# Kernel optimization log

Measured on AMD Instinct MI355X. Metric: run time of the kernel, lower is better.

The kernel has to match this reference:

```python
import jax, jax.numpy as jnp
import numpy as np

K = 3
STRIDE = 1
PAD = 1


def conv2d(x, w, b):
    # standard NCHW conv, stride 1, pad 1
    out = jax.lax.conv_general_dilated(
        x, w, (STRIDE, STRIDE), [(PAD, PAD), (PAD, PAD)],
        dimension_numbers=("NCHW", "OIHW", "NCHW"))
    return out + b[None, :, None, None]


def deform_conv2d(x, offset, mask, weight):
    # torchvision.ops.deform_conv2d semantics (offset_groups=1):
    # offset: [B, 2*K*K, Ho, Wo] laid out as (k, (y, x)) per kernel tap k (row-major)
    # mask:   [B, K*K, Ho, Wo]
    B, C, H, W = x.shape
    KK = K * K
    Ho, Wo = offset.shape[2:]
    off = offset.reshape(B, KK, 2, Ho, Wo)

    # base sampling positions: p = out*stride - pad + kernel_tap + offset
    tap_y = jnp.repeat(jnp.arange(K, dtype=x.dtype), K)  # [KK]
    tap_x = jnp.tile(jnp.arange(K, dtype=x.dtype), K)    # [KK]
    grid_y = jnp.arange(Ho, dtype=x.dtype) * STRIDE - PAD
    grid_x = jnp.arange(Wo, dtype=x.dtype) * STRIDE - PAD
    py = grid_y[None, None, :, None] + tap_y[None, :, None, None] + off[:, :, 0]  # [B,KK,Ho,Wo]
    px = grid_x[None, None, None, :] + tap_x[None, :, None, None] + off[:, :, 1]

    y0 = jnp.floor(py)
    x0 = jnp.floor(px)
    wy1 = py - y0  # fractional parts
    wx1 = px - x0

    xf = x.reshape(B, C, H * W)

    def gather(yi, xi):
        # zero-padding semantics: out-of-bounds corners contribute 0
        valid = (yi >= 0) & (yi <= H - 1) & (xi >= 0) & (xi <= W - 1)
        idx = (jnp.clip(yi, 0, H - 1) * W + jnp.clip(xi, 0, W - 1)).astype(jnp.int32)
        v = jnp.take_along_axis(xf, idx.reshape(B, 1, KK * Ho * Wo), axis=2)
        v = v.reshape(B, C, KK, Ho, Wo)
        return v * valid[:, None].astype(x.dtype)

    e = lambda a: a[:, None]  # [B,KK,Ho,Wo] -> [B,1,KK,Ho,Wo]
    sampled = (gather(y0, x0) * e((1 - wy1) * (1 - wx1))
               + gather(y0, x0 + 1) * e((1 - wy1) * wx1)
               + gather(y0 + 1, x0) * e(wy1 * (1 - wx1))
               + gather(y0 + 1, x0 + 1) * e(wy1 * wx1))
    sampled = sampled * mask[:, None]  # modulated, [B,C,KK,Ho,Wo]

    Cout = weight.shape[0]
    out = jnp.einsum("bckhw,ock->bohw", sampled, weight.reshape(Cout, C, KK))
    return out


def setup_inputs() -> dict:
    key = jax.random.key(0)
    ks = jax.random.split(key, 5)
    B, Cin, Cout, H, W = 4, 128, 256, 64, 64
    x = jax.random.normal(ks[0], (B, Cin, H, W), jnp.float32)
    # offset/modulator convs are zero-init in the module; use small random weights
    # so the deformable sampling path is actually exercised
    offset_w = jax.random.normal(ks[1], (2 * K * K, Cin, K, K), jnp.float32) * 0.02
    offset_b = jax.random.normal(ks[2], (2 * K * K,), jnp.float32) * 0.1
    mod_w = jax.random.normal(ks[3], (K * K, Cin, K, K), jnp.float32) * 0.02
    mod_b = jnp.zeros((K * K,), jnp.float32)
    weight = jax.random.normal(ks[4], (Cout, Cin, K, K), jnp.float32) * (1.0 / np.sqrt(Cin * K * K))
    return {"x": x, "offset_w": offset_w, "offset_b": offset_b,
            "mod_w": mod_w, "mod_b": mod_b, "weight": weight}


def reference(x, offset_w, offset_b, mod_w, mod_b, weight):
    H, W = x.shape[2], x.shape[3]
    max_offset = max(H, W) / 4.0
    offset = jnp.clip(conv2d(x, offset_w, offset_b), -max_offset, max_offset)
    mask = 2.0 * jax.nn.sigmoid(conv2d(x, mod_w, mod_b))
    return deform_conv2d(x, offset, mask, weight)
```

## Files before the change

### kernel.cpp

```cpp
#include <hip/hip_runtime.h>
#include <math.h>

#define CIN   128
#define COUT  256
#define HH    64
#define WW    64
#define BB    4
#define KK    9
#define CK    (CIN*KK)

typedef unsigned short u16;
typedef unsigned int   u32;
using f32x4  = __attribute__((ext_vector_type(4))) float;
using s16x8  = __attribute__((ext_vector_type(8))) short;

__device__ __forceinline__ u16 f2bf(float f) {
    union { float f; u32 u; } v; v.f = f;
    u32 u = v.u;
    u += 0x7FFFu + ((u >> 16) & 1u);
    return (u16)(u >> 16);
}
__device__ __forceinline__ float bfel(s16x8 v, int j) {
    union { u32 u; float f; } c; c.u = ((u32)(u16)v[j]) << 16; return c.f;
}
__device__ __forceinline__ u32 asu(float f) {
    union { float f; u32 u; } v; v.f = f; return v.u;
}

__global__ __launch_bounds__(256)
void prep_all(const float* __restrict__ x, const float* __restrict__ w,
              const float* __restrict__ ow, const float* __restrict__ mw,
              u16* __restrict__ xt, u16* __restrict__ wfrag,
              u16* __restrict__ wofsf) {
    __shared__ u16 T[64][130];
    int blk = blockIdx.x;
    int tid = threadIdx.x;

    if (blk < 256) {
        int b = blk >> 6, y = blk & 63;
        int lane = tid & 63, cw = tid >> 6;
        for (int c = cw; c < 128; c += 4)
            T[lane][c] = f2bf(x[((b * 128 + c) * 64 + y) * 64 + lane]);
        __syncthreads();
        int c = tid & 127;
        for (int p = tid >> 7; p < 64; p += 2)
            xt[((b * 64 + y) * 64 + p) * 128 + c] = T[p][c];
    } else if (blk < 256 + 1152) {
        int i = (blk - 256) * 256 + tid;
        int j    = i & 7;
        int lane = (i >> 3) & 63;
        int ks4  = (i >> 9) & 3;
        int t    = (i >> 11) & 1;
        int wv   = (i >> 12) & 7;
        int tap  = i >> 15;
        int co = (wv * 2 + t) * 16 + (lane & 15);
        int k  = tap * 128 + ks4 * 32 + (lane >> 4) * 8 + j;
        int c  = k & 127;
        wfrag[i] = f2bf(w[co * CK + c * 9 + tap]);
    } else {
        int i = (blk - 1408) * 256 + tid;
        if (i < 9 * 4096) {
            int j    = i & 7;
            int lane = (i >> 3) & 63;
            int ks4  = (i >> 9) & 3;
            int t    = (i >> 11) & 1;
            int tap  = i >> 12;
            int co = t * 16 + (lane & 15);
            int k  = tap * 128 + ks4 * 32 + (lane >> 4) * 8 + j;
            int c  = k & 127;
            float v = 0.f;
            if (co < 18)      v = ow[co * CK + c * 9 + tap];
            else if (co < 27) v = mw[(co - 18) * CK + c * 9 + tap];
            wofsf[i] = f2bf(v);
        }
    }
}

__global__ __launch_bounds__(512, 4)
void dcn_fused(const u16* __restrict__ xt, const u16* __restrict__ wofsf,
               const float* __restrict__ ob, const float* __restrict__ mb,
               const u16* __restrict__ wfrag, float* __restrict__ out) {
    int blkid = blockIdx.x;
    int xcd = blkid & 7, idx = blkid >> 3;
    int b   = xcd >> 1;
    int ho  = ((xcd & 1) << 5) + (idx >> 1);
    int wo0 = (idx & 1) << 5;
    int tid = threadIdx.x;

    __shared__ __align__(16) u16 Sm[4][32][136];
    __shared__ float s_om[27][32];
    __shared__ int   s_idx[32][KK][4];
    __shared__ float s_wgt[32][KK][4];

    int wv   = tid >> 6, lane = tid & 63;
    int quad = lane >> 4, l16 = lane & 15;
    int gpx  = wv * 4 + (lane >> 4);
    int oct  = lane & 15;

    const u16* xtb = xt + (size_t)b * 4096 * 128;
    const s16x8 vzero = {0,0,0,0,0,0,0,0};

    if (wv < 4) {
        int t  = wv & 1;
        int ph = wv >> 1;
        f32x4 aco = (f32x4)(0.f);
        int col0 = wo0 + ph * 16 + l16 - 1;
#pragma unroll
        for (int tap = 0; tap < KK; ++tap) {
            int y   = ho - 1 + tap / 3;
            int col = col0 + tap % 3;
            bool ok = ((unsigned)y < HH) && ((unsigned)col < WW);
            int yc = ((unsigned)y < HH) ? y : 0;
            int cc = ((unsigned)col < WW) ? col : 0;
            const u16* src = xtb + (size_t)(yc * 64 + cc) * 128 + quad * 8;
            const u16* wc  = wofsf + tap * 4096 + t * 2048 + lane * 8;
#pragma unroll
            for (int ks4 = 0; ks4 < 4; ++ks4) {
                s16x8 bf = *(const s16x8*)(src + ks4 * 32);
                bf = ok ? bf : vzero;
                s16x8 af = *(const s16x8*)(wc + ks4 * 512);
                aco = __builtin_amdgcn_mfma_f32_16x16x32_bf16(af, bf, aco, 0, 0, 0);
            }
        }
#pragma unroll
        for (int r = 0; r < 4; ++r) {
            int co = t * 16 + quad * 4 + r;
            if (co < 27) {
                float v = aco[r];
                if (co < 18) {
                    v += ob[co];
                    v = fminf(fmaxf(v, -16.f), 16.f);
                } else {
                    v += mb[co - 18];
                    v = 2.f / (1.f + expf(-v));
                }
                s_om[co][ph * 16 + l16] = v;
            }
        }
    }
    __syncthreads();

    if (tid < 32 * KK) {
        int p = tid / KK, k = tid - (tid / KK) * KK;
        int wo = wo0 + p;
        float offy = s_om[2 * k][p];
        float offx = s_om[2 * k + 1][p];
        float mval = s_om[18 + k][p];

        float py = (float)(ho - 1 + k / 3) + offy;
        float px = (float)(wo - 1 + k % 3) + offx;
        float y0f = floorf(py), x0f = floorf(px);
        float wy1 = py - y0f,  wx1 = px - x0f;
        float wy0 = 1.f - wy1, wx0 = 1.f - wx1;
        int iy0 = (int)y0f, ix0 = (int)x0f;
        int iy1 = iy0 + 1,  ix1 = ix0 + 1;
        bool vy0 = (iy0 >= 0) && (iy0 < HH);
        bool vy1 = (iy1 >= 0) && (iy1 < HH);
        bool vx0 = (ix0 >= 0) && (ix0 < WW);
        bool vx1 = (ix1 >= 0) && (ix1 < WW);
        int cy0 = min(max(iy0, 0), HH - 1), cy1 = min(max(iy1, 0), HH - 1);
        int cx0 = min(max(ix0, 0), WW - 1), cx1 = min(max(ix1, 0), WW - 1);
        s_idx[p][k][0] = (cy0 * WW + cx0) * 128;
        s_idx[p][k][1] = (cy0 * WW + cx1) * 128;
        s_idx[p][k][2] = (cy1 * WW + cx0) * 128;
        s_idx[p][k][3] = (cy1 * WW + cx1) * 128;
        s_wgt[p][k][0] = (vy0 && vx0) ? mval * wy0 * wx0 : 0.f;
        s_wgt[p][k][1] = (vy0 && vx1) ? mval * wy0 * wx1 : 0.f;
        s_wgt[p][k][2] = (vy1 && vx0) ? mval * wy1 * wx0 : 0.f;
        s_wgt[p][k][3] = (vy1 && vx1) ? mval * wy1 * wx1 : 0.f;
    }
    __syncthreads();

    f32x4 acc[2][2];
#pragma unroll
    for (int t = 0; t < 2; ++t) { acc[t][0] = (f32x4)(0.f); acc[t][1] = (f32x4)(0.f); }

    s16x8 crs[2][2][4];
    float gs[2][2][4];
    auto gatherB = [&](int tap, int sp, int ti) {
        int i0 = s_idx[gpx][tap][0], i1 = s_idx[gpx][tap][1];
        int i2 = s_idx[gpx][tap][2], i3 = s_idx[gpx][tap][3];
        gs[sp][ti][0] = s_wgt[gpx][tap][0]; gs[sp][ti][1] = s_wgt[gpx][tap][1];
        gs[sp][ti][2] = s_wgt[gpx][tap][2]; gs[sp][ti][3] = s_wgt[gpx][tap][3];
        int co8 = oct * 8;
        crs[sp][ti][0] = *(const s16x8*)(xtb + i0 + co8);
        crs[sp][ti][1] = *(const s16x8*)(xtb + i1 + co8);
        crs[sp][ti][2] = *(const s16x8*)(xtb + i2 + co8);
        crs[sp][ti][3] = *(const s16x8*)(xtb + i3 + co8);
    };

    auto blend_store = [&](int sp, int ti, int slot) {
        float g0 = gs[sp][ti][0], g1 = gs[sp][ti][1];
        float g2 = gs[sp][ti][2], g3 = gs[sp][ti][3];
        float o[8];
#pragma unroll
        for (int j = 0; j < 8; ++j)
            o[j] = g0 * bfel(crs[sp][ti][0], j) + g1 * bfel(crs[sp][ti][1], j)
                 + g2 * bfel(crs[sp][ti][2], j) + g3 * bfel(crs[sp][ti][3], j);
        uint4 pkv;
        pkv.x = (asu(o[1]) & 0xFFFF0000u) | (asu(o[0]) >> 16);
        pkv.y = (asu(o[3]) & 0xFFFF0000u) | (asu(o[2]) >> 16);
        pkv.z = (asu(o[5]) & 0xFFFF0000u) | (asu(o[4]) >> 16);
        pkv.w = (asu(o[7]) & 0xFFFF0000u) | (asu(o[6]) >> 16);
        *(uint4*)(&Sm[slot][gpx][oct * 8]) = pkv;
    };

    auto pb_mfma_tap = [&](int tap, int slot) {
        const u16* wc = wfrag + (tap * 8 + wv) * 4096 + lane * 8;
        s16x8 af[8];
#pragma unroll
        for (int t = 0; t < 2; ++t)
#pragma unroll
            for (int ks4 = 0; ks4 < 4; ++ks4)
                af[t * 4 + ks4] = *(const s16x8*)(wc + (t * 4 + ks4) * 512);
#pragma unroll
        for (int ks4 = 0; ks4 < 4; ++ks4) {
            s16x8 bf0 = *(const s16x8*)(&Sm[slot][l16][ks4 * 32 + quad * 8]);
            s16x8 bf1 = *(const s16x8*)(&Sm[slot][16 + l16][ks4 * 32 + quad * 8]);
#pragma unroll
            for (int t = 0; t < 2; ++t) {
                acc[t][0] = __builtin_amdgcn_mfma_f32_16x16x32_bf16(af[t * 4 + ks4], bf0, acc[t][0], 0, 0, 0);
                acc[t][1] = __builtin_amdgcn_mfma_f32_16x16x32_bf16(af[t * 4 + ks4], bf1, acc[t][1], 0, 0, 0);
            }
        }
    };

    gatherB(0, 0, 0);
    gatherB(1, 0, 1);
#pragma unroll
    for (int p = 0; p < 4; ++p) {
        int sp = p & 1;
        blend_store(sp, 0, 2 * sp);
        blend_store(sp, 1, 2 * sp + 1);
        __syncthreads();
        if (p < 3) { gatherB(2 * p + 2, sp ^ 1, 0); gatherB(2 * p + 3, sp ^ 1, 1); }
        else       { gatherB(8,         sp ^ 1, 0); }
        pb_mfma_tap(2 * p,     2 * sp);
        pb_mfma_tap(2 * p + 1, 2 * sp + 1);
    }
    blend_store(0, 0, 0);
    __syncthreads();
    pb_mfma_tap(8, 0);

#pragma unroll
    for (int t = 0; t < 2; ++t) {
        int cobase = (wv * 2 + t) * 16 + quad * 4;
#pragma unroll
        for (int ph = 0; ph < 2; ++ph) {
#pragma unroll
            for (int r = 0; r < 4; ++r) {
                int co = cobase + r;
                out[((b * COUT + co) * HH + ho) * WW + wo0 + ph * 16 + l16] = acc[t][ph][r];
            }
        }
    }
}

extern "C" void kernel_launch(void* const* d_in, const int* in_sizes, int n_in,
                              void* d_out, int out_size, void* d_ws, size_t ws_size,
                              hipStream_t stream) {
    const float* x  = (const float*)d_in[0];
    const float* ow = (const float*)d_in[1];
    const float* ob = (const float*)d_in[2];
    const float* mw = (const float*)d_in[3];
    const float* mb = (const float*)d_in[4];
    const float* wt = (const float*)d_in[5];

    char* ws = (char*)d_ws;
    u16* wfrag = (u16*)ws;  ws += (size_t)COUT * CK * 2;
    u16* wofsf = (u16*)ws;  ws += (size_t)32 * CK * 2;
    u16* xt    = (u16*)ws;
    float* out = (float*)d_out;

    prep_all<<<1552, 256, 0, stream>>>(x, wt, ow, mw, xt, wfrag, wofsf);

    dcn_fused<<<BB * HH * 2, 512, 0, stream>>>(xt, wofsf, ob, mb, wfrag, out);
}
```

Measured before the change: 105.4 us.

## Process a full output row per block to halve weight-fragment reloads

Each block now covers an entire 64-pixel output row instead of half a row, so the grid shrinks from 512 to 256 blocks. Every weight fragment loaded from global memory is reused across four pixel tiles instead of two, halving total weight traffic. The pipeline also changes from two taps per stage to one tap per stage over double-buffered shared memory, with weight fragments prefetched before the barrier, and all eight waves now compute the offset/mask convolution. In exchange there are fewer blocks (256 on a 256-CU part, one wave of blocks), more accumulator registers, and lower occupancy (launch bounds 2).

```diff
diff --git a/kernel.cpp b/kernel.cpp
--- a/kernel.cpp
+++ b/kernel.cpp
@@ -76,35 +76,33 @@
     }
 }
 
-__global__ __launch_bounds__(512, 4)
+__global__ __launch_bounds__(512, 2)
 void dcn_fused(const u16* __restrict__ xt, const u16* __restrict__ wofsf,
                const float* __restrict__ ob, const float* __restrict__ mb,
                const u16* __restrict__ wfrag, float* __restrict__ out) {
     int blkid = blockIdx.x;
     int xcd = blkid & 7, idx = blkid >> 3;
     int b   = xcd >> 1;
-    int ho  = ((xcd & 1) << 5) + (idx >> 1);
-    int wo0 = (idx & 1) << 5;
+    int ho  = ((xcd & 1) << 5) + idx;
     int tid = threadIdx.x;
 
-    __shared__ __align__(16) u16 Sm[4][32][136];
-    __shared__ float s_om[27][32];
-    __shared__ int   s_idx[32][KK][4];
-    __shared__ float s_wgt[32][KK][4];
+    __shared__ __align__(16) u16 Sm[2][64][136];
+    __shared__ float s_om[27][64];
+    __shared__ int   s_idx[64][KK][4];
+    __shared__ float s_wgt[64][KK][4];
 
     int wv   = tid >> 6, lane = tid & 63;
     int quad = lane >> 4, l16 = lane & 15;
-    int gpx  = wv * 4 + (lane >> 4);
-    int oct  = lane & 15;
+    int p2   = (wv * 4 + quad) * 2;
 
     const u16* xtb = xt + (size_t)b * 4096 * 128;
     const s16x8 vzero = {0,0,0,0,0,0,0,0};
 
-    if (wv < 4) {
+    {
         int t  = wv & 1;
         int ph = wv >> 1;
         f32x4 aco = (f32x4)(0.f);
-        int col0 = wo0 + ph * 16 + l16 - 1;
+        int col0 = ph * 16 + l16 - 1;
 #pragma unroll
         for (int tap = 0; tap < KK; ++tap) {
             int y   = ho - 1 + tap / 3;
@@ -140,9 +138,9 @@
     }
     __syncthreads();
 
-    if (tid < 32 * KK) {
-        int p = tid / KK, k = tid - (tid / KK) * KK;
-        int wo = wo0 + p;
+    for (int i = tid; i < 64 * KK; i += 512) {
+        int p = i / KK, k = i - (i / KK) * KK;
+        int wo = p;
         float offy = s_om[2 * k][p];
         float offx = s_om[2 * k + 1][p];
         float mval = s_om[18 + k][p];
@@ -171,86 +169,95 @@
     }
     __syncthreads();
 
-    f32x4 acc[2][2];
-#pragma unroll
-    for (int t = 0; t < 2; ++t) { acc[t][0] = (f32x4)(0.f); acc[t][1] = (f32x4)(0.f); }
+    f32x4 acc[2][4];
+#pragma unroll
+    for (int t = 0; t < 2; ++t)
+#pragma unroll
+        for (int ph = 0; ph < 4; ++ph) acc[t][ph] = (f32x4)(0.f);
 
     s16x8 crs[2][2][4];
     float gs[2][2][4];
-    auto gatherB = [&](int tap, int sp, int ti) {
-        int i0 = s_idx[gpx][tap][0], i1 = s_idx[gpx][tap][1];
-        int i2 = s_idx[gpx][tap][2], i3 = s_idx[gpx][tap][3];
-        gs[sp][ti][0] = s_wgt[gpx][tap][0]; gs[sp][ti][1] = s_wgt[gpx][tap][1];
-        gs[sp][ti][2] = s_wgt[gpx][tap][2]; gs[sp][ti][3] = s_wgt[gpx][tap][3];
-        int co8 = oct * 8;
-        crs[sp][ti][0] = *(const s16x8*)(xtb + i0 + co8);
-        crs[sp][ti][1] = *(const s16x8*)(xtb + i1 + co8);
-        crs[sp][ti][2] = *(const s16x8*)(xtb + i2 + co8);
-        crs[sp][ti][3] = *(const s16x8*)(xtb + i3 + co8);
-    };
-
-    auto blend_store = [&](int sp, int ti, int slot) {
-        float g0 = gs[sp][ti][0], g1 = gs[sp][ti][1];
-        float g2 = gs[sp][ti][2], g3 = gs[sp][ti][3];
-        float o[8];
-#pragma unroll
-        for (int j = 0; j < 8; ++j)
-            o[j] = g0 * bfel(crs[sp][ti][0], j) + g1 * bfel(crs[sp][ti][1], j)
-                 + g2 * bfel(crs[sp][ti][2], j) + g3 * bfel(crs[sp][ti][3], j);
-        uint4 pkv;
-        pkv.x = (asu(o[1]) & 0xFFFF0000u) | (asu(o[0]) >> 16);
-        pkv.y = (asu(o[3]) & 0xFFFF0000u) | (asu(o[2]) >> 16);
-        pkv.z = (asu(o[5]) & 0xFFFF0000u) | (asu(o[4]) >> 16);
-        pkv.w = (asu(o[7]) & 0xFFFF0000u) | (asu(o[6]) >> 16);
-        *(uint4*)(&Sm[slot][gpx][oct * 8]) = pkv;
-    };
-
-    auto pb_mfma_tap = [&](int tap, int slot) {
+    s16x8 afp[8];
+
+    auto gatherB = [&](int tap, int sp) {
+#pragma unroll
+        for (int e = 0; e < 2; ++e) {
+            int p = p2 + e;
+            int i0 = s_idx[p][tap][0], i1 = s_idx[p][tap][1];
+            int i2 = s_idx[p][tap][2], i3 = s_idx[p][tap][3];
+            gs[sp][e][0] = s_wgt[p][tap][0]; gs[sp][e][1] = s_wgt[p][tap][1];
+            gs[sp][e][2] = s_wgt[p][tap][2]; gs[sp][e][3] = s_wgt[p][tap][3];
+            int co8 = l16 * 8;
+            crs[sp][e][0] = *(const s16x8*)(xtb + i0 + co8);
+            crs[sp][e][1] = *(const s16x8*)(xtb + i1 + co8);
+            crs[sp][e][2] = *(const s16x8*)(xtb + i2 + co8);
+            crs[sp][e][3] = *(const s16x8*)(xtb + i3 + co8);
+        }
+    };
+
+    auto blend_store = [&](int sp) {
+#pragma unroll
+        for (int e = 0; e < 2; ++e) {
+            float g0 = gs[sp][e][0], g1 = gs[sp][e][1];
+            float g2 = gs[sp][e][2], g3 = gs[sp][e][3];
+            float o[8];
+#pragma unroll
+            for (int j = 0; j < 8; ++j)
+                o[j] = g0 * bfel(crs[sp][e][0], j) + g1 * bfel(crs[sp][e][1], j)
+                     + g2 * bfel(crs[sp][e][2], j) + g3 * bfel(crs[sp][e][3], j);
+            uint4 pkv;
+            pkv.x = (asu(o[1]) & 0xFFFF0000u) | (asu(o[0]) >> 16);
+            pkv.y = (asu(o[3]) & 0xFFFF0000u) | (asu(o[2]) >> 16);
+            pkv.z = (asu(o[5]) & 0xFFFF0000u) | (asu(o[4]) >> 16);
+            pkv.w = (asu(o[7]) & 0xFFFF0000u) | (asu(o[6]) >> 16);
+            *(uint4*)(&Sm[sp][p2 + e][l16 * 8]) = pkv;
+        }
+    };
+
+    auto af_prefetch = [&](int tap) {
         const u16* wc = wfrag + (tap * 8 + wv) * 4096 + lane * 8;
-        s16x8 af[8];
 #pragma unroll
         for (int t = 0; t < 2; ++t)
 #pragma unroll
             for (int ks4 = 0; ks4 < 4; ++ks4)
-                af[t * 4 + ks4] = *(const s16x8*)(wc + (t * 4 + ks4) * 512);
+                afp[t * 4 + ks4] = *(const s16x8*)(wc + (t * 4 + ks4) * 512);
+    };
+
+    auto pb_mfma_tap = [&](int sp) {
 #pragma unroll
         for (int ks4 = 0; ks4 < 4; ++ks4) {
-            s16x8 bf0 = *(const s16x8*)(&Sm[slot][l16][ks4 * 32 + quad * 8]);
-            s16x8 bf1 = *(const s16x8*)(&Sm[slot][16 + l16][ks4 * 32 + quad * 8]);
-#pragma unroll
-            for (int t = 0; t < 2; ++t) {
-                acc[t][0] = __builtin_amdgcn_mfma_f32_16x16x32_bf16(af[t * 4 + ks4], bf0, acc[t][0], 0, 0, 0);
-                acc[t][1] = __builtin_amdgcn_mfma_f32_16x16x32_bf16(af[t * 4 + ks4], bf1, acc[t][1], 0, 0, 0);
-            }
-        }
-    };
-
-    gatherB(0, 0, 0);
-    gatherB(1, 0, 1);
-#pragma unroll
-    for (int p = 0; p < 4; ++p) {
-        int sp = p & 1;
-        blend_store(sp, 0, 2 * sp);
-        blend_store(sp, 1, 2 * sp + 1);
+            s16x8 bf[4];
+#pragma unroll
+            for (int ph = 0; ph < 4; ++ph)
+                bf[ph] = *(const s16x8*)(&Sm[sp][ph * 16 + l16][ks4 * 32 + quad * 8]);
+#pragma unroll
+            for (int t = 0; t < 2; ++t)
+#pragma unroll
+                for (int ph = 0; ph < 4; ++ph)
+                    acc[t][ph] = __builtin_amdgcn_mfma_f32_16x16x32_bf16(afp[t * 4 + ks4], bf[ph], acc[t][ph], 0, 0, 0);
+        }
+    };
+
+    gatherB(0, 0);
+#pragma unroll
+    for (int tap = 0; tap < KK; ++tap) {
+        int sp = tap & 1;
+        blend_store(sp);
+        af_prefetch(tap);
         __syncthreads();
-        if (p < 3) { gatherB(2 * p + 2, sp ^ 1, 0); gatherB(2 * p + 3, sp ^ 1, 1); }
-        else       { gatherB(8,         sp ^ 1, 0); }
-        pb_mfma_tap(2 * p,     2 * sp);
-        pb_mfma_tap(2 * p + 1, 2 * sp + 1);
-    }
-    blend_store(0, 0, 0);
-    __syncthreads();
-    pb_mfma_tap(8, 0);
+        if (tap < KK - 1) gatherB(tap + 1, sp ^ 1);
+        pb_mfma_tap(sp);
+    }
 
 #pragma unroll
     for (int t = 0; t < 2; ++t) {
         int cobase = (wv * 2 + t) * 16 + quad * 4;
 #pragma unroll
-        for (int ph = 0; ph < 2; ++ph) {
+        for (int ph = 0; ph < 4; ++ph) {
 #pragma unroll
             for (int r = 0; r < 4; ++r) {
                 int co = cobase + r;
-                out[((b * COUT + co) * HH + ho) * WW + wo0 + ph * 16 + l16] = acc[t][ph][r];
+                out[((b * COUT + co) * HH + ho) * WW + ph * 16 + l16] = acc[t][ph][r];
             }
         }
     }
@@ -274,5 +281,5 @@
 
     prep_all<<<1552, 256, 0, stream>>>(x, wt, ow, mw, xt, wfrag, wofsf);
 
-    dcn_fused<<<BB * HH * 2, 512, 0, stream>>>(xt, wofsf, ob, mb, wfrag, out);
-}
+    dcn_fused<<<BB * HH, 512, 0, stream>>>(xt, wofsf, ob, mb, wfrag, out);
+}
```

After: 101.8 us, median of 2. -3.4%, faster.
